# Kernel optimization log

Measured on AMD Instinct MI355X. Metric: run time of the kernel, lower is better.

The kernel has to match this reference:

```python
import jax, jax.numpy as jnp
import numpy as np

SEQ_LEN, BATCH, TAGS = 512, 1024, 32
START_IDX, END_IDX = 30, 31
NEG = -10000.0


def setup_inputs() -> dict:
    key = jax.random.key(0)
    k1, k2 = jax.random.split(key)
    feats = jax.random.normal(k1, (SEQ_LEN, BATCH, TAGS), dtype=jnp.float32)
    mask = jnp.ones((SEQ_LEN, BATCH), dtype=jnp.float32)
    # xavier-normal-ish transition, then apply START/END constraints as in reset_parameters
    transition = jax.random.normal(k2, (TAGS, TAGS), dtype=jnp.float32) * (2.0 / (TAGS + TAGS)) ** 0.5
    transition = transition.at[START_IDX, :].set(NEG)
    transition = transition.at[:, END_IDX].set(NEG)
    return {"feats": feats, "mask": mask, "transition": transition}


def reference(feats, mask, transition):
    # feats: (T, N, M), mask: (T, N), transition: (M, M)
    batch_size, tag_size = feats.shape[1], feats.shape[2]
    alpha0 = jnp.full((batch_size, tag_size), NEG, dtype=feats.dtype)
    alpha0 = alpha0.at[:, START_IDX].set(0.0)

    def step(alpha, inp):
        feat_t, mask_t = inp  # (N, M), (N,)
        # score[n, j, i] = alpha[n, i] + transition[j, i] + feat[n, j]
        score = alpha[:, None, :] + transition[None, :, :] + feat_t[:, :, None]
        new_alpha = jax.nn.logsumexp(score, axis=-1)  # (N, M)
        m = mask_t[:, None]
        alpha = new_alpha * m + alpha * (1.0 - m)
        return alpha, None

    alpha, _ = jax.lax.scan(step, alpha0, (feats, mask))
    alpha = alpha + transition[END_IDX][None, :]
    return jax.nn.logsumexp(alpha, axis=-1)  # (N,)
```

## Files before the change

kernel.cpp:

```cpp
#include <hip/hip_runtime.h>


constexpr int SEQ = 512, BATCH = 1024, TAGS = 32;
constexpr int HALF = SEQ / 2;
constexpr int D = 16;

#define LOG2E 1.4426950408889634f
#define LN2   0.6931471805599453f

typedef __attribute__((ext_vector_type(8))) short short8;
typedef __attribute__((ext_vector_type(4))) float float4v;
union Frag8 { unsigned u[4]; short8 v; };

__device__ __forceinline__ unsigned pk_rn(float x, float y) {
  return __builtin_amdgcn_perm(__float_as_uint(y) + 0x8000u,
                               __float_as_uint(x) + 0x8000u, 0x07060302u);
}
__device__ __forceinline__ unsigned pk_tr(float x, float y) {
  return __builtin_amdgcn_perm(__float_as_uint(y), __float_as_uint(x), 0x07060302u);
}

template <bool FWD>
__device__ __forceinline__ void run_chain(
    const float* __restrict__ feats, const float* __restrict__ maskp,
    const float* __restrict__ trans, float* __restrict__ out,
    float* __restrict__ vbuf, float* __restrict__ c2buf, int b0, int lane) {
  const int s = lane & 15, q = lane >> 4;

  const size_t fstep = (size_t)BATCH * TAGS;
  const ptrdiff_t fs = FWD ? (ptrdiff_t)fstep : -(ptrdiff_t)fstep;
  const ptrdiff_t ms = FWD ? (ptrdiff_t)BATCH : -(ptrdiff_t)BATCH;
  const float* pLo = feats + (size_t)(b0 + s) * TAGS + 4 * q +
                     (FWD ? 0 : (size_t)(SEQ - 1) * fstep);
  const float* pHi = pLo + 16;
  const float* pM = maskp + b0 + s + (FWD ? 0 : (size_t)(SEQ - 1) * BATCH);

  float4v Rlo[D], Rhi[D];
  float Rm[D];
#pragma unroll
  for (int d = 0; d < D; ++d) {
    Rlo[d] = *(const float4v*)(pLo + (ptrdiff_t)d * fs);
    Rhi[d] = *(const float4v*)(pHi + (ptrdiff_t)d * fs);
    Rm[d] = *(pM + (ptrdiff_t)d * ms);
  }

  int sig[8];
#pragma unroll
  for (int i = 0; i < 8; ++i) sig[i] = (i < 4) ? (4 * q + i) : (16 + 4 * q + (i - 4));
  Frag8 e0, e1;
#pragma unroll
  for (int p = 0; p < 4; ++p) {
    if (FWD) {
      e0.u[p] = pk_rn(__builtin_amdgcn_exp2f(trans[s * TAGS + sig[2 * p]] * LOG2E),
                      __builtin_amdgcn_exp2f(trans[s * TAGS + sig[2 * p + 1]] * LOG2E));
      e1.u[p] = pk_rn(__builtin_amdgcn_exp2f(trans[(16 + s) * TAGS + sig[2 * p]] * LOG2E),
                      __builtin_amdgcn_exp2f(trans[(16 + s) * TAGS + sig[2 * p + 1]] * LOG2E));
    } else {
      e0.u[p] = pk_rn(__builtin_amdgcn_exp2f(trans[sig[2 * p] * TAGS + s] * LOG2E),
                      __builtin_amdgcn_exp2f(trans[sig[2 * p + 1] * TAGS + s] * LOG2E));
      e1.u[p] = pk_rn(__builtin_amdgcn_exp2f(trans[sig[2 * p] * TAGS + 16 + s] * LOG2E),
                      __builtin_amdgcn_exp2f(trans[sig[2 * p + 1] * TAGS + 16 + s] * LOG2E));
    }
  }

  float a[8];
#pragma unroll
  for (int i = 0; i < 8; ++i) {
    if (FWD) a[i] = (q == 3 && i == 6) ? 1.0f : 0.0f;
    else a[i] = __builtin_amdgcn_exp2f(
        trans[31 * TAGS + ((i < 4) ? (4 * q + i) : (16 + 4 * q + (i - 4)))] * LOG2E);
  }
  Frag8 Bf;
  Bf.u[0] = pk_tr(a[0], a[1]); Bf.u[1] = pk_tr(a[2], a[3]);
  Bf.u[2] = pk_tr(a[4], a[5]); Bf.u[3] = pk_tr(a[6], a[7]);
  float c2 = 0.f;
  const float4v zerov = {0.f, 0.f, 0.f, 0.f};

  float4v Fc0, Fc1;
  float mc;
#pragma unroll
  for (int i = 0; i < 4; ++i) {
    Fc0[i] = __builtin_amdgcn_exp2f(Rlo[0][i] * LOG2E);
    Fc1[i] = __builtin_amdgcn_exp2f(Rhi[0][i] * LOG2E);
  }
  mc = Rm[0];

  for (int g = 0; g < HALF / D; ++g) {
    const bool issue = (g < HALF / D - 1);
    const float* qLo = pLo + (ptrdiff_t)(g + 1) * D * fs;
    const float* qHi = qLo + 16;
    const float* qM = pM + (ptrdiff_t)(g + 1) * D * ms;
#pragma unroll
    for (int u = 0; u < D; ++u) {
      if (issue) {
        Rlo[u] = *(const float4v*)(qLo + (ptrdiff_t)u * fs);
        Rhi[u] = *(const float4v*)(qHi + (ptrdiff_t)u * fs);
        Rm[u] = *(qM + (ptrdiff_t)u * ms);
      }

      const bool mv = (mc != 0.0f);
      if (FWD) {
        const float4v D0 = __builtin_amdgcn_mfma_f32_16x16x32_bf16(e0.v, Bf.v, zerov, 0, 0, 0);
        const float4v D1 = __builtin_amdgcn_mfma_f32_16x16x32_bf16(e1.v, Bf.v, zerov, 0, 0, 0);
#pragma unroll
        for (int i = 0; i < 4; ++i) {
          a[i] = mv ? D0[i] * Fc0[i] : a[i];
          a[4 + i] = mv ? D1[i] * Fc1[i] : a[4 + i];
        }
      } else {
        float tb[8];
#pragma unroll
        for (int i = 0; i < 4; ++i) { tb[i] = a[i] * Fc0[i]; tb[4 + i] = a[4 + i] * Fc1[i]; }
        Frag8 Bp;
        Bp.u[0] = pk_tr(tb[0], tb[1]); Bp.u[1] = pk_tr(tb[2], tb[3]);
        Bp.u[2] = pk_tr(tb[4], tb[5]); Bp.u[3] = pk_tr(tb[6], tb[7]);
        const float4v D0 = __builtin_amdgcn_mfma_f32_16x16x32_bf16(e0.v, Bp.v, zerov, 0, 0, 0);
        const float4v D1 = __builtin_amdgcn_mfma_f32_16x16x32_bf16(e1.v, Bp.v, zerov, 0, 0, 0);
#pragma unroll
        for (int i = 0; i < 4; ++i) {
          a[i] = mv ? D0[i] : a[i];
          a[4 + i] = mv ? D1[i] : a[4 + i];
        }
      }

      if ((u & 7) == 7) {
        float mx = fmaxf(fmaxf(fmaxf(a[0], a[1]), fmaxf(a[2], a[3])),
                         fmaxf(fmaxf(a[4], a[5]), fmaxf(a[6], a[7])));
        mx = fmaxf(mx, __shfl_xor(mx, 16, 64));
        mx = fmaxf(mx, __shfl_xor(mx, 32, 64));
        const int ex = (int)((__float_as_uint(mx) >> 23) & 0xFFu) - 127;
        const float scl = __uint_as_float((unsigned)(127 - ex) << 23);
#pragma unroll
        for (int i = 0; i < 8; ++i) a[i] *= scl;
        c2 += (float)ex;
      }

      if (FWD) {
        Bf.u[0] = pk_tr(a[0], a[1]); Bf.u[1] = pk_tr(a[2], a[3]);
        Bf.u[2] = pk_tr(a[4], a[5]); Bf.u[3] = pk_tr(a[6], a[7]);
      }

      const int nu = (u + 1) & (D - 1);
#pragma unroll
      for (int i = 0; i < 4; ++i) {
        Fc0[i] = __builtin_amdgcn_exp2f(Rlo[nu][i] * LOG2E);
        Fc1[i] = __builtin_amdgcn_exp2f(Rhi[nu][i] * LOG2E);
      }
      mc = Rm[nu];
    }
  }

  if (!FWD) {
    float4v lo = {a[0], a[1], a[2], a[3]}, hi = {a[4], a[5], a[6], a[7]};
    *(float4v*)(vbuf + lane * 8) = lo;
    *(float4v*)(vbuf + lane * 8 + 4) = hi;
    if (lane < 16) c2buf[lane] = c2;
  }
  __syncthreads();
  if (FWD) {
    const float4v v0 = *(const float4v*)(vbuf + lane * 8);
    const float4v v1 = *(const float4v*)(vbuf + lane * 8 + 4);
    float dot = a[0] * v0[0] + a[1] * v0[1] + a[2] * v0[2] + a[3] * v0[3] +
                a[4] * v1[0] + a[5] * v1[1] + a[6] * v1[2] + a[7] * v1[3];
    dot += __shfl_xor(dot, 16, 64);
    dot += __shfl_xor(dot, 32, 64);
    if (lane < 16)
      out[b0 + lane] = LN2 * (c2 + c2buf[lane] + __builtin_amdgcn_logf(dot));
  }
}

extern "C" __global__ void __launch_bounds__(128, 1) crf_scan(
    const float* __restrict__ feats, const float* __restrict__ mask,
    const float* __restrict__ trans, float* __restrict__ out) {
  __shared__ float vbuf[512];
  __shared__ float c2buf[16];
  const int wid = threadIdx.x >> 6;
  const int lane = threadIdx.x & 63;
  const int b0 = blockIdx.x * 16;
  if (wid == 0)
    run_chain<true>(feats, mask, trans, out, vbuf, c2buf, b0, lane);
  else
    run_chain<false>(feats, mask, trans, out, vbuf, c2buf, b0, lane);
}

extern "C" void kernel_launch(void* const* d_in, const int* in_sizes, int n_in,
                              void* d_out, int out_size, void* d_ws, size_t ws_size,
                              hipStream_t stream) {
  const float* feats = (const float*)d_in[0];
  const float* mask  = (const float*)d_in[1];
  const float* trans = (const float*)d_in[2];
  float* out = (float*)d_out;
  hipLaunchKernelGGL(crf_scan, dim3(BATCH / 16), dim3(128), 0, stream,
                     feats, mask, trans, out);
}
```

Baseline: 120.6 us.

## Add producer warps streaming feats into double-buffered LDS via global_load_lds

Splits each block into two consumer waves that run the forward and backward chains and two producer waves that prefetch feats and mask chunks of 8 steps into double-buffered LDS, using direct global-to-LDS loads with an XOR swizzle. The consumers drop their large register prefetch arrays and read from LDS instead. The aim is to free registers and keep memory latency off the serial recurrence. In exchange it adds a block-wide barrier per chunk, which ties the two chains and the producers together in lockstep, plus LDS read latency on the critical path.

```diff
diff --git a/kernel.cpp b/kernel.cpp
--- a/kernel.cpp
+++ b/kernel.cpp
@@ -2,8 +2,10 @@
 
 
 constexpr int SEQ = 512, BATCH = 1024, TAGS = 32;
-constexpr int HALF = SEQ / 2;
-constexpr int D = 16;
+constexpr int CH = 8;
+constexpr int NCH = (SEQ / 2) / CH;
+constexpr int FSLOT = CH * 512;
+constexpr int MSLOT = CH * 16;
 
 #define LOG2E 1.4426950408889634f
 #define LN2   0.6931471805599453f
@@ -20,29 +22,58 @@
   return __builtin_amdgcn_perm(__float_as_uint(y), __float_as_uint(x), 0x07060302u);
 }
 
+__device__ __forceinline__ void gld16(const float* g, float* l) {
+  __builtin_amdgcn_global_load_lds((const __attribute__((address_space(1))) void*)g,
+                                   (__attribute__((address_space(3))) void*)l, 16, 0, 0);
+}
+__device__ __forceinline__ void gld4(const float* g, float* l) {
+  __builtin_amdgcn_global_load_lds((const __attribute__((address_space(1))) void*)g,
+                                   (__attribute__((address_space(3))) void*)l, 4, 0, 0);
+}
+
 template <bool FWD>
-__device__ __forceinline__ void run_chain(
+__device__ __forceinline__ void produce(
     const float* __restrict__ feats, const float* __restrict__ maskp,
+    float* __restrict__ FFd, float* __restrict__ MMd, int b0, int lane) {
+  const int bs = lane >> 3;
+  const int tg = 4 * ((lane & 7) ^ (bs & 7));
+  const size_t t0 = FWD ? 0 : (size_t)(SEQ - 1);
+  const float* gF0 = feats + t0 * BATCH * TAGS + (size_t)(b0 + bs) * TAGS + tg;
+  const float* gF8 = gF0 + 8 * TAGS;
+  const float* gM0 = maskp +
+      (FWD ? (size_t)(lane >> 4) : (size_t)(SEQ - 1 - (lane >> 4))) * BATCH +
+      b0 + (lane & 15);
+  const ptrdiff_t fstep = FWD ? (ptrdiff_t)(BATCH * TAGS) : -(ptrdiff_t)(BATCH * TAGS);
+  const ptrdiff_t mstep = FWD ? (ptrdiff_t)BATCH : -(ptrdiff_t)BATCH;
+
+  auto FILL = [&](int k) {
+    float* fb = FFd + (k & 1) * FSLOT;
+    float* mb = MMd + (k & 1) * MSLOT;
+#pragma unroll
+    for (int j = 0; j < CH; ++j) {
+      const ptrdiff_t o = (ptrdiff_t)(CH * k + j) * fstep;
+      gld16(gF0 + o, fb + j * 512);
+      gld16(gF8 + o, fb + j * 512 + 256);
+    }
+    gld4(gM0 + (ptrdiff_t)(CH * k) * mstep, mb);
+    gld4(gM0 + (ptrdiff_t)(CH * k + 4) * mstep, mb + 64);
+  };
+
+  FILL(0);
+  __syncthreads();
+  for (int k = 0; k < NCH; ++k) {
+    if (k < NCH - 1) FILL(k + 1);
+    __syncthreads();
+  }
+  __syncthreads();
+}
+
+template <bool FWD>
+__device__ __forceinline__ void consume(
     const float* __restrict__ trans, float* __restrict__ out,
+    const float* __restrict__ FFd, const float* __restrict__ MMd,
     float* __restrict__ vbuf, float* __restrict__ c2buf, int b0, int lane) {
   const int s = lane & 15, q = lane >> 4;
-
-  const size_t fstep = (size_t)BATCH * TAGS;
-  const ptrdiff_t fs = FWD ? (ptrdiff_t)fstep : -(ptrdiff_t)fstep;
-  const ptrdiff_t ms = FWD ? (ptrdiff_t)BATCH : -(ptrdiff_t)BATCH;
-  const float* pLo = feats + (size_t)(b0 + s) * TAGS + 4 * q +
-                     (FWD ? 0 : (size_t)(SEQ - 1) * fstep);
-  const float* pHi = pLo + 16;
-  const float* pM = maskp + b0 + s + (FWD ? 0 : (size_t)(SEQ - 1) * BATCH);
-
-  float4v Rlo[D], Rhi[D];
-  float Rm[D];
-#pragma unroll
-  for (int d = 0; d < D; ++d) {
-    Rlo[d] = *(const float4v*)(pLo + (ptrdiff_t)d * fs);
-    Rhi[d] = *(const float4v*)(pHi + (ptrdiff_t)d * fs);
-    Rm[d] = *(pM + (ptrdiff_t)d * ms);
-  }
 
   int sig[8];
 #pragma unroll
@@ -76,29 +107,25 @@
   float c2 = 0.f;
   const float4v zerov = {0.f, 0.f, 0.f, 0.f};
 
-  float4v Fc0, Fc1;
-  float mc;
-#pragma unroll
-  for (int i = 0; i < 4; ++i) {
-    Fc0[i] = __builtin_amdgcn_exp2f(Rlo[0][i] * LOG2E);
-    Fc1[i] = __builtin_amdgcn_exp2f(Rhi[0][i] * LOG2E);
-  }
-  mc = Rm[0];
-
-  for (int g = 0; g < HALF / D; ++g) {
-    const bool issue = (g < HALF / D - 1);
-    const float* qLo = pLo + (ptrdiff_t)(g + 1) * D * fs;
-    const float* qHi = qLo + 16;
-    const float* qM = pM + (ptrdiff_t)(g + 1) * D * ms;
-#pragma unroll
-    for (int u = 0; u < D; ++u) {
-      if (issue) {
-        Rlo[u] = *(const float4v*)(qLo + (ptrdiff_t)u * fs);
-        Rhi[u] = *(const float4v*)(qHi + (ptrdiff_t)u * fs);
-        Rm[u] = *(qM + (ptrdiff_t)u * ms);
-      }
-
-      const bool mv = (mc != 0.0f);
+  const int off0 = s * 32 + ((q ^ (s & 7)) << 2);
+  const int off1 = s * 32 + (((q + 4) ^ (s & 7)) << 2);
+
+  __syncthreads();
+  for (int k = 0; k < NCH; ++k) {
+    const float* fb = FFd + (k & 1) * FSLOT;
+    const float* mb = MMd + (k & 1) * MSLOT;
+#pragma unroll
+    for (int j = 0; j < CH; ++j) {
+      const float4v r0 = *(const float4v*)(fb + j * 512 + off0);
+      const float4v r1 = *(const float4v*)(fb + j * 512 + off1);
+      const float mval = mb[j * 16 + s];
+      float4v Fc0, Fc1;
+#pragma unroll
+      for (int i = 0; i < 4; ++i) {
+        Fc0[i] = __builtin_amdgcn_exp2f(r0[i] * LOG2E);
+        Fc1[i] = __builtin_amdgcn_exp2f(r1[i] * LOG2E);
+      }
+      const bool mv = (mval != 0.0f);
       if (FWD) {
         const float4v D0 = __builtin_amdgcn_mfma_f32_16x16x32_bf16(e0.v, Bf.v, zerov, 0, 0, 0);
         const float4v D1 = __builtin_amdgcn_mfma_f32_16x16x32_bf16(e1.v, Bf.v, zerov, 0, 0, 0);
@@ -122,8 +149,7 @@
           a[4 + i] = mv ? D1[i] : a[4 + i];
         }
       }
-
-      if ((u & 7) == 7) {
+      if (j == CH - 1) {
         float mx = fmaxf(fmaxf(fmaxf(a[0], a[1]), fmaxf(a[2], a[3])),
                          fmaxf(fmaxf(a[4], a[5]), fmaxf(a[6], a[7])));
         mx = fmaxf(mx, __shfl_xor(mx, 16, 64));
@@ -134,20 +160,12 @@
         for (int i = 0; i < 8; ++i) a[i] *= scl;
         c2 += (float)ex;
       }
-
       if (FWD) {
         Bf.u[0] = pk_tr(a[0], a[1]); Bf.u[1] = pk_tr(a[2], a[3]);
         Bf.u[2] = pk_tr(a[4], a[5]); Bf.u[3] = pk_tr(a[6], a[7]);
       }
-
-      const int nu = (u + 1) & (D - 1);
-#pragma unroll
-      for (int i = 0; i < 4; ++i) {
-        Fc0[i] = __builtin_amdgcn_exp2f(Rlo[nu][i] * LOG2E);
-        Fc1[i] = __builtin_amdgcn_exp2f(Rhi[nu][i] * LOG2E);
-      }
-      mc = Rm[nu];
     }
+    __syncthreads();
   }
 
   if (!FWD) {
@@ -169,18 +187,25 @@
   }
 }
 
-extern "C" __global__ void __launch_bounds__(128, 1) crf_scan(
+extern "C" __global__ void __launch_bounds__(256, 1) crf_scan(
     const float* __restrict__ feats, const float* __restrict__ mask,
     const float* __restrict__ trans, float* __restrict__ out) {
+  __shared__ float FF[2][2][FSLOT];
+  __shared__ float MM[2][2][MSLOT];
   __shared__ float vbuf[512];
   __shared__ float c2buf[16];
   const int wid = threadIdx.x >> 6;
   const int lane = threadIdx.x & 63;
   const int b0 = blockIdx.x * 16;
+
   if (wid == 0)
-    run_chain<true>(feats, mask, trans, out, vbuf, c2buf, b0, lane);
+    consume<true>(trans, out, &FF[0][0][0], &MM[0][0][0], vbuf, c2buf, b0, lane);
+  else if (wid == 1)
+    consume<false>(trans, out, &FF[1][0][0], &MM[1][0][0], vbuf, c2buf, b0, lane);
+  else if (wid == 2)
+    produce<true>(feats, mask, &FF[0][0][0], &MM[0][0][0], b0, lane);
   else
-    run_chain<false>(feats, mask, trans, out, vbuf, c2buf, b0, lane);
+    produce<false>(feats, mask, &FF[1][0][0], &MM[1][0][0], b0, lane);
 }
 
 extern "C" void kernel_launch(void* const* d_in, const int* in_sizes, int n_in,
@@ -190,6 +215,6 @@
   const float* mask  = (const float*)d_in[1];
   const float* trans = (const float*)d_in[2];
   float* out = (float*)d_out;
-  hipLaunchKernelGGL(crf_scan, dim3(BATCH / 16), dim3(128), 0, stream,
+  hipLaunchKernelGGL(crf_scan, dim3(BATCH / 16), dim3(256), 0, stream,
                      feats, mask, trans, out);
 }
```

New measurement: 117.4 us. 2.7% less time.
